# Kernel optimization log

Hardware: AMD Instinct MI355X
Metric: run time of the kernel (lower is better)

## Reference

```python
import jax, jax.numpy as jnp
import numpy as np

N, E, D, L = 32768, 65536, 128, 8

def setup_inputs() -> dict:
    key = jax.random.key(0)
    ks = jax.random.split(key, 32)
    def rn(i, shape, s=0.05):
        return jax.random.normal(ks[i], shape, dtype=jnp.float32) * s
    inp = dict(
        hs_init=rn(0, (N, D), 1.0),
        edge_index=jax.random.randint(ks[1], (2, E), 0, N, dtype=jnp.int32),
        gate=jax.random.randint(ks[2], (N,), 0, 3, dtype=jnp.int32),
        level=jax.random.randint(ks[3], (N,), 0, L + 1, dtype=jnp.int32),
        gcn_w=rn(4, (D, D)), gcn_b=rn(5, (D,)),
        mu_w=rn(6, (D, D)), mu_b=rn(7, (D,)),
        ls_w=rn(8, (D, D)), ls_b=rn(9, (D,)),
        as_w=rn(10, (D, D)), as_b=rn(11, (D,)),
        ns_w=rn(12, (D, D)), ns_b=rn(13, (D,)),
        af_w=rn(14, (2 * D, D)), af_b=rn(15, (D,)),
        nf_w=rn(16, (D, D)), nf_b=rn(17, (D,)),
        ua_w=rn(18, (2 * D, D)), ua_b=rn(19, (D,)),
        un_w=rn(20, (D, D)), un_b=rn(21, (D,)),
        dec_ws=rn(22, (D, D)), dec_wt=rn(23, (D, D)),
    )
    return inp

def reference(hs_init, edge_index, gate, level, gcn_w, gcn_b, mu_w, mu_b, ls_w, ls_b,
              as_w, as_b, ns_w, ns_b, af_w, af_b, nf_w, nf_b, ua_w, ua_b, un_w, un_b,
              dec_ws, dec_wt):
    seg = jax.ops.segment_sum
    src, dst = edge_index[0], edge_index[1]
    n = hs_init.shape[0]
    hs = hs_init                       # structural embedding [N, D]
    hf = jnp.zeros_like(hs)            # functional embedding [N, D]
    and_mask = gate == 1
    not_mask = gate == 2
    # --- GCN encoder (self-loops, symmetric in-degree normalization) ---
    x = hs @ gcn_w
    deg = seg(jnp.ones_like(src, dtype=x.dtype), dst, num_segments=n) + 1.0
    dis = jax.lax.rsqrt(deg)
    coef = (dis[src] * dis[dst])[:, None]
    x = seg(coef * x[src], dst, num_segments=n) + (1.0 / deg)[:, None] * x + gcn_b
    # --- VAE head: eval mode -> hs = mu (logstd computed as in module, unused) ---
    mu = x @ mu_w + mu_b
    logstd = jnp.minimum(x @ ls_w + ls_b, 10.0)  # MAX_LOGSTD clamp, eval-mode unused
    hs = mu
    # --- level-wise propagation: gather -> MLP aggr (sum) -> masked scatter update ---
    for l in range(1, L + 1):
        lvl = level == l
        # AND gates at this level
        m_and = and_mask & lvl
        e_and = m_and[dst].astype(hs.dtype)[:, None]   # edges targeting level-l ANDs
        msg = jax.nn.relu(hs @ as_w + as_b)
        agg = seg(e_and * msg[src], dst, num_segments=n)
        hs_and = jax.nn.relu(jnp.concatenate([hs, agg], axis=1) @ ua_w + ua_b)
        hs = jnp.where(m_and[:, None], hs_and, hs)
        fmsg = jax.nn.relu(jnp.concatenate([hs, hf], axis=1) @ af_w + af_b)
        fagg = seg(e_and * fmsg[src], dst, num_segments=n)
        hf = jnp.where(m_and[:, None], fagg, hf)
        # NOT gates at this level
        m_not = not_mask & lvl
        e_not = m_not[dst].astype(hs.dtype)[:, None]
        msg = jax.nn.relu(hs @ ns_w + ns_b)
        agg = seg(e_not * msg[src], dst, num_segments=n)
        hs_not = jnp.tanh(agg @ un_w + un_b)
        hs = jnp.where(m_not[:, None], hs_not, hs)
        fmsg = jax.nn.relu(hf @ nf_w + nf_b)
        fagg = seg(e_not * fmsg[src], dst, num_segments=n)
        hf = jnp.where(m_not[:, None], fagg, hf)
    # --- directed inner-product decoder -> node-level functional embedding ---
    zs = hs @ dec_ws
    zt = hs @ dec_wt
    w = jax.nn.sigmoid(jnp.sum(zs[src] * zt[dst], axis=-1))[:, None]  # [E,1]
    hf = seg(w * zs[src], dst, num_segments=n)
    return hs, hf
```

## Files before the change

### kernel.cpp

```cpp
#include <hip/hip_runtime.h>

#define DIM 128
#define NLEV 8
#define NB_STAGE 512
#define NSLOT (NB_STAGE * 4)
#define CAP NSLOT

#define AS4 0
#define UA4 4096
#define NS4 12288
#define UN4 16384
#define PACK4_TOTAL 20480
#define DEC_TOTAL 16384

__device__ __forceinline__ int cls_of(int g, int l) {
    if (l < 1 || l > NLEV) return -1;
    if (g == 1) return l - 1;
    if (g == 2) return NLEV + (l - 1);
    return -1;
}


__global__ __launch_bounds__(256) void count_kernel(const int* __restrict__ dstv,
                                                    int* __restrict__ degi, int E,
                                                    const int* __restrict__ gate,
                                                    const int* __restrict__ level,
                                                    int* __restrict__ nlist,
                                                    int* __restrict__ ncnt,
                                                    int* __restrict__ clsidx, int n) {
    const int i = blockIdx.x * 256 + threadIdx.x;
    if (i < E) atomicAdd(&degi[dstv[i]], 1);
    if ((int)blockIdx.x * 256 < n) {
        __shared__ int lcnt[16];
        __shared__ int lbase[16];
        const int t = threadIdx.x;
        if (t < 16) lcnt[t] = 0;
        __syncthreads();
        int c = -1, lpos = 0;
        if (i < n) {
            c = cls_of(gate[i], level[i]);
            if (c >= 0) lpos = atomicAdd(&lcnt[c], 1);
        }
        __syncthreads();
        if (t < 16 && lcnt[t] > 0) lbase[t] = atomicAdd(&ncnt[t], lcnt[t]);
        __syncthreads();
        if (c >= 0) {
            int idx = lbase[c] + lpos;
            nlist[c * n + idx] = i;
            clsidx[i] = (c << 16) | idx;
        }
    }
}

__global__ void pack_kernel(const float* __restrict__ as_w, const float* __restrict__ ua_w,
                            const float* __restrict__ ns_w, const float* __restrict__ un_w,
                            float4* __restrict__ wp4,
                            const float* __restrict__ ws_w, const float* __restrict__ wt_w,
                            float2* __restrict__ wdec,
                            const float* __restrict__ gcn_b, const float* __restrict__ mu_w,
                            const float* __restrict__ mu_b, float* __restrict__ bp) {
    if (blockIdx.x == gridDim.x - 1) {
        const int j = threadIdx.x;
        if (j < DIM) {
            float acc = mu_b[j];
            for (int k = 0; k < DIM; k++) acc = fmaf(gcn_b[k], mu_w[k * DIM + j], acc);
            bp[j] = acc;
        }
        return;
    }
    const int i = blockIdx.x * 256 + threadIdx.x;
    if (i < PACK4_TOTAL) {
        const float* src;
        int local;
        if (i < UA4)      { src = as_w; local = i; }
        else if (i < NS4) { src = ua_w; local = i - UA4; }
        else if (i < UN4) { src = ns_w; local = i - NS4; }
        else              { src = un_w; local = i - UN4; }
        const int kp = local >> 6, jl = local & 63;
        wp4[i] = make_float4(src[(2 * kp) * DIM + jl], src[(2 * kp) * DIM + jl + 64],
                             src[(2 * kp + 1) * DIM + jl], src[(2 * kp + 1) * DIM + jl + 64]);
    } else if (i < PACK4_TOTAL + DEC_TOTAL) {
        const int d = i - PACK4_TOTAL;
        wdec[d] = make_float2(ws_w[d], wt_w[d]);
    }
}

__global__ __launch_bounds__(1024) void scan1_kernel(const int* __restrict__ degi,
                                                     int* __restrict__ offs,
                                                     int* __restrict__ bsum,
                                                     float* __restrict__ dis,
                                                     float* __restrict__ inv) {
    __shared__ int sh[1024];
    const int gid = blockIdx.x * 1024 + threadIdx.x;
    const int v = degi[gid];
    {
        float d = (float)v + 1.0f;
        dis[gid] = rsqrtf(d);
        inv[gid] = 1.0f / d;
    }
    sh[threadIdx.x] = v;
    __syncthreads();
    for (int off = 1; off < 1024; off <<= 1) {
        int t = (threadIdx.x >= off) ? sh[threadIdx.x - off] : 0;
        __syncthreads();
        sh[threadIdx.x] += t;
        __syncthreads();
    }
    offs[gid] = sh[threadIdx.x] - v;
    if (threadIdx.x == 1023) bsum[blockIdx.x] = sh[1023];
}

__global__ __launch_bounds__(1024) void scan3_kernel(int* __restrict__ offs,
                                                     const int* __restrict__ bsum, int n) {
    __shared__ int sbase, stot;
    const int nb = gridDim.x;
    if (threadIdx.x < 64) {
        const int lane = threadIdx.x;
        const int orig = (lane < nb) ? bsum[lane] : 0;
        int v = orig;
#pragma unroll
        for (int off = 1; off < 64; off <<= 1) {
            int t = __shfl_up(v, off, 64);
            if (lane >= off) v += t;
        }
        if (lane == (int)blockIdx.x) sbase = v - orig;
        if (lane == nb - 1) stot = v;
    }
    __syncthreads();
    const int gid = blockIdx.x * 1024 + threadIdx.x;
    offs[gid] += sbase;
    if (gid == n - 1) offs[n] = stot;
}

__global__ void csr_fill_kernel(const int* __restrict__ srcv, const int* __restrict__ dstv,
                                const int* __restrict__ offs, int* __restrict__ cursor,
                                int* __restrict__ csr_src, int E) {
    int i = blockIdx.x * blockDim.x + threadIdx.x;
    if (i >= E) return;
    int d = dstv[i];
    int pos = offs[d] + atomicAdd(&cursor[d], 1);
    csr_src[pos] = srcv[i];
}

template <int BIAS>
__global__ __launch_bounds__(256) void mm_kernel(const float* __restrict__ in0,
                                                 const float* __restrict__ W,
                                                 const float* __restrict__ b,
                                                 float* __restrict__ out, int n) {
    const int R = 32;
    __shared__ float tile[R * DIM];
    const size_t row0 = (size_t)blockIdx.x * R;
    for (int t = threadIdx.x; t < R * DIM / 4; t += 256)
        ((float4*)tile)[t] = ((const float4*)(in0 + row0 * DIM))[t];
    __syncthreads();
    const int g = threadIdx.x >> 7;
    const int j = threadIdx.x & 127;
    float acc[16];
#pragma unroll
    for (int r = 0; r < 16; r++) acc[r] = 0.f;
    const float* tb = tile + (g * 16) * DIM;
    for (int k = 0; k < DIM; k += 4) {
        float w0 = W[(k + 0) * DIM + j];
        float w1 = W[(k + 1) * DIM + j];
        float w2 = W[(k + 2) * DIM + j];
        float w3 = W[(k + 3) * DIM + j];
#pragma unroll
        for (int r = 0; r < 16; r++) {
            const float4 a = *reinterpret_cast<const float4*>(tb + r * DIM + k);
            acc[r] = fmaf(a.x, w0, acc[r]);
            acc[r] = fmaf(a.y, w1, acc[r]);
            acc[r] = fmaf(a.z, w2, acc[r]);
            acc[r] = fmaf(a.w, w3, acc[r]);
        }
    }
    float bias = BIAS ? b[j] : 0.f;
#pragma unroll
    for (int r = 0; r < 16; r++) out[(row0 + g * 16 + r) * DIM + j] = acc[r] + bias;
}

__global__ __launch_bounds__(256) void mm2_kernel(const float* __restrict__ in0,
                                                  const float2* __restrict__ Wd,
                                                  float* __restrict__ zs,
                                                  float* __restrict__ zt, int n) {
    const int R = 32;
    __shared__ float tile[R * DIM];
    const size_t row0 = (size_t)blockIdx.x * R;
    for (int t = threadIdx.x; t < R * DIM / 4; t += 256)
        ((float4*)tile)[t] = ((const float4*)(in0 + row0 * DIM))[t];
    __syncthreads();
    const int g = threadIdx.x >> 7;
    const int j = threadIdx.x & 127;
    float accs[16], acct[16];
#pragma unroll
    for (int r = 0; r < 16; r++) { accs[r] = 0.f; acct[r] = 0.f; }
    const float* tb = tile + (g * 16) * DIM;
    float2 s0 = Wd[0 * DIM + j], s1 = Wd[1 * DIM + j];
    float2 s2 = Wd[2 * DIM + j], s3 = Wd[3 * DIM + j];
    for (int k = 0; k < DIM; k += 2) {
        const int kn = (k + 4 < DIM) ? (k + 4) : 0;
        const float2 p0 = Wd[(kn + 0) * DIM + j];
        const float2 p1 = Wd[(kn + 1) * DIM + j];
#pragma unroll
        for (int r = 0; r < 16; r++) {
            const float2 a = *reinterpret_cast<const float2*>(tb + r * DIM + k);
            accs[r] = fmaf(a.x, s0.x, accs[r]);
            acct[r] = fmaf(a.x, s0.y, acct[r]);
            accs[r] = fmaf(a.y, s1.x, accs[r]);
            acct[r] = fmaf(a.y, s1.y, acct[r]);
        }
        s0 = s2; s1 = s3; s2 = p0; s3 = p1;
    }
#pragma unroll
    for (int r = 0; r < 16; r++) {
        zs[(row0 + g * 16 + r) * DIM + j] = accs[r];
        zt[(row0 + g * 16 + r) * DIM + j] = acct[r];
    }
}

__global__ __launch_bounds__(256) void gcn_gather_kernel(const float* __restrict__ x,
                                                         const float* __restrict__ dis,
                                                         const float* __restrict__ inv,
                                                         const int* __restrict__ offs,
                                                         const int* __restrict__ csr_src,
                                                         float* __restrict__ y, int n) {
    int slot = threadIdx.x >> 7, j = threadIdx.x & 127;
    for (int node = blockIdx.x * 2 + slot; node < n; node += gridDim.x * 2) {
        float di = dis[node];
        float acc = inv[node] * x[(size_t)node * DIM + j];
        int e1 = offs[node + 1];
        for (int p = offs[node]; p < e1; p++) {
            int s = csr_src[p];
            acc += di * dis[s] * x[(size_t)s * DIM + j];
        }
        y[(size_t)node * DIM + j] = acc;
    }
}


__device__ __forceinline__ void stage_pk(const float4* __restrict__ Wp, float4* __restrict__ W2) {
    for (int t = threadIdx.x; t < 4096; t += 256) W2[t] = Wp[t];
}

template <bool MERGE>
__device__ __forceinline__ const float* resolve_row(const float* __restrict__ base,
                                                    const float* __restrict__ tmp,
                                                    const int* __restrict__ clsidx,
                                                    int mcls, int s) {
    if (MERGE) {
        int cc = clsidx[s];
        if ((cc >> 16) == mcls && (cc & 0xFFFF) < CAP) return tmp + (size_t)(cc & 0xFFFF) * DIM;
    }
    return base + (size_t)s * DIM;
}

template <bool MERGE>
__device__ __forceinline__ void load_pair(const float* __restrict__ hs,
                                          const float* __restrict__ tmp,
                                          const int* __restrict__ clsidx, int mcls,
                                          const int* __restrict__ csr_src,
                                          int p, int e1, int lane,
                                          float& a00, float& a01, float& a10, float& a11) {
    const int s0 = csr_src[p];
    const int s1 = (p + 1 < e1) ? csr_src[p + 1] : s0;
    const float* r0 = resolve_row<MERGE>(hs, tmp, clsidx, mcls, s0);
    const float* r1 = resolve_row<MERGE>(hs, tmp, clsidx, mcls, s1);
    a00 = r0[lane]; a01 = r0[lane + 64];
    a10 = r1[lane]; a11 = r1[lane + 64];
}

__device__ __forceinline__ void mv128(const float* __restrict__ ar, const float4* __restrict__ W2,
                                      int lane, float& o0, float& o1) {
#pragma unroll 8
    for (int k = 0; k < 128; k += 4) {
        const float4 a = *(const float4*)&ar[k];
        const float4 wA = W2[(k >> 1) * 64 + lane];
        const float4 wB = W2[((k >> 1) + 1) * 64 + lane];
        o0 = fmaf(a.x, wA.x, o0); o1 = fmaf(a.x, wA.y, o1);
        o0 = fmaf(a.y, wA.z, o0); o1 = fmaf(a.y, wA.w, o1);
        o0 = fmaf(a.z, wB.x, o0); o1 = fmaf(a.z, wB.y, o1);
        o0 = fmaf(a.w, wB.z, o0); o1 = fmaf(a.w, wB.w, o1);
    }
}

template <bool MERGE>
__global__ __launch_bounds__(256) void and_stage_kernel(
        float* __restrict__ hs, const float* __restrict__ tmpN, float* __restrict__ tmpA,
        const int* __restrict__ offs, const int* __restrict__ csr_src,
        const int* __restrict__ nlist, const int* __restrict__ ncnt,
        const int* __restrict__ clsidx, const float4* __restrict__ wp4,
        const float* __restrict__ as_b, const float* __restrict__ ua_b,
        int cA, int cNp, int n) {
    const int cnt = min(ncnt[cA], CAP);
    const int cntp = MERGE ? min(ncnt[cNp], CAP) : 0;
    const int lim = max(cnt, cntp);
    if ((int)blockIdx.x * 4 >= lim) return;
    __shared__ float4 W2[4096];
    __shared__ float arow[4][256];
    const int lane = threadIdx.x & 63;
    const int wv = threadIdx.x >> 6;
    const int gslot = (blockIdx.x << 2) | wv;

    const bool act = gslot < cnt;
    const int nd = act ? nlist[cA * n + gslot] : 0;
    const int e0 = act ? offs[nd] : 0;
    const int e1 = act ? offs[nd + 1] : 0;
    float h0 = 0.f, h1 = 0.f;
    if (act) {
        h0 = hs[(size_t)nd * DIM + lane];
        h1 = hs[(size_t)nd * DIM + lane + 64];
    }
    float pa0 = 0.f, pa1 = 0.f, pa2 = 0.f, pa3 = 0.f;
    if (act && e0 < e1)
        load_pair<MERGE>(hs, tmpN, clsidx, cNp, csr_src, e0, e1, lane, pa0, pa1, pa2, pa3);
    if (MERGE) {
        for (int idx = gslot; idx < cntp; idx += NSLOT) {
            const int node = nlist[cNp * n + idx];
            hs[(size_t)node * DIM + lane] = tmpN[(size_t)idx * DIM + lane];
            hs[(size_t)node * DIM + lane + 64] = tmpN[(size_t)idx * DIM + lane + 64];
        }
    }
    stage_pk(wp4 + AS4, W2);
    __syncthreads();

    const float bj_as0 = as_b[lane], bj_as1 = as_b[lane + 64];
    float ag0 = 0.f, ag1 = 0.f;
    if (act) {
        float* ar = arow[wv];
        float a00 = pa0, a01 = pa1, a10 = pa2, a11 = pa3;
        for (int p = e0; p < e1; p += 2) {
            ar[lane] = a00; ar[64 + lane] = a01;
            ar[128 + lane] = a10; ar[192 + lane] = a11;
            const bool two = (p + 1 < e1);
            float n00 = 0.f, n01 = 0.f, n10 = 0.f, n11 = 0.f;
            if (p + 2 < e1)
                load_pair<MERGE>(hs, tmpN, clsidx, cNp, csr_src, p + 2, e1, lane,
                                 n00, n01, n10, n11);
            float m00 = bj_as0, m01 = bj_as1, m10 = bj_as0, m11 = bj_as1;
#pragma unroll 8
            for (int k = 0; k < 128; k += 4) {
                const float4 a0 = *(const float4*)&ar[k];
                const float4 a1 = *(const float4*)&ar[128 + k];
                const float4 wA = W2[(k >> 1) * 64 + lane];
                const float4 wB = W2[((k >> 1) + 1) * 64 + lane];
                m00 = fmaf(a0.x, wA.x, m00); m01 = fmaf(a0.x, wA.y, m01);
                m10 = fmaf(a1.x, wA.x, m10); m11 = fmaf(a1.x, wA.y, m11);
                m00 = fmaf(a0.y, wA.z, m00); m01 = fmaf(a0.y, wA.w, m01);
                m10 = fmaf(a1.y, wA.z, m10); m11 = fmaf(a1.y, wA.w, m11);
                m00 = fmaf(a0.z, wB.x, m00); m01 = fmaf(a0.z, wB.y, m01);
                m10 = fmaf(a1.z, wB.x, m10); m11 = fmaf(a1.z, wB.y, m11);
                m00 = fmaf(a0.w, wB.z, m00); m01 = fmaf(a0.w, wB.w, m01);
                m10 = fmaf(a1.w, wB.z, m10); m11 = fmaf(a1.w, wB.w, m11);
            }
            ag0 += fmaxf(m00, 0.f);
            ag1 += fmaxf(m01, 0.f);
            if (two) { ag0 += fmaxf(m10, 0.f); ag1 += fmaxf(m11, 0.f); }
            a00 = n00; a01 = n01; a10 = n10; a11 = n11;
        }
    }

    float u0 = ua_b[lane], u1 = ua_b[lane + 64];
    __syncthreads();
    stage_pk(wp4 + UA4, W2);
    __syncthreads();
    if (act) {
        float* ar = arow[wv];
        ar[lane] = h0; ar[64 + lane] = h1;
        mv128(ar, W2, lane, u0, u1);
    }
    __syncthreads();
    stage_pk(wp4 + UA4 + 4096, W2);
    __syncthreads();
    if (act) {
        float* ar = arow[wv];
        ar[lane] = ag0; ar[64 + lane] = ag1;
        mv128(ar, W2, lane, u0, u1);
        tmpA[(size_t)gslot * DIM + lane] = fmaxf(u0, 0.f);
        tmpA[(size_t)gslot * DIM + lane + 64] = fmaxf(u1, 0.f);
    }
}

__global__ __launch_bounds__(256) void not_stage_kernel(
        float* __restrict__ hs, const float* __restrict__ tmpA, float* __restrict__ tmpN,
        const int* __restrict__ offs, const int* __restrict__ csr_src,
        const int* __restrict__ nlist, const int* __restrict__ ncnt,
        const int* __restrict__ clsidx, const float4* __restrict__ wp4,
        const float* __restrict__ ns_b, const float* __restrict__ un_b,
        int cA, int cN, int n) {
    const int cnt = min(ncnt[cN], CAP);
    const int cntA = min(ncnt[cA], CAP);
    const int lim = max(cnt, cntA);
    if ((int)blockIdx.x * 4 >= lim) return;
    __shared__ float4 W2[4096];
    __shared__ float arow[4][256];
    const int lane = threadIdx.x & 63;
    const int wv = threadIdx.x >> 6;
    const int gslot = (blockIdx.x << 2) | wv;

    const bool act = gslot < cnt;
    const int nd = act ? nlist[cN * n + gslot] : 0;
    const int e0 = act ? offs[nd] : 0;
    const int e1 = act ? offs[nd + 1] : 0;
    float pa0 = 0.f, pa1 = 0.f, pa2 = 0.f, pa3 = 0.f;
    if (act && e0 < e1)
        load_pair<true>(hs, tmpA, clsidx, cA, csr_src, e0, e1, lane, pa0, pa1, pa2, pa3);
    for (int idx = gslot; idx < cntA; idx += NSLOT) {
        const int node = nlist[cA * n + idx];
        hs[(size_t)node * DIM + lane] = tmpA[(size_t)idx * DIM + lane];
        hs[(size_t)node * DIM + lane + 64] = tmpA[(size_t)idx * DIM + lane + 64];
    }
    stage_pk(wp4 + NS4, W2);
    __syncthreads();

    const float bj_ns0 = ns_b[lane], bj_ns1 = ns_b[lane + 64];
    float ag0 = 0.f, ag1 = 0.f;
    if (act) {
        float* ar = arow[wv];
        float a00 = pa0, a01 = pa1, a10 = pa2, a11 = pa3;
        for (int p = e0; p < e1; p += 2) {
            ar[lane] = a00; ar[64 + lane] = a01;
            ar[128 + lane] = a10; ar[192 + lane] = a11;
            const bool two = (p + 1 < e1);
            float n00 = 0.f, n01 = 0.f, n10 = 0.f, n11 = 0.f;
            if (p + 2 < e1)
                load_pair<true>(hs, tmpA, clsidx, cA, csr_src, p + 2, e1, lane,
                                n00, n01, n10, n11);
            float m00 = bj_ns0, m01 = bj_ns1, m10 = bj_ns0, m11 = bj_ns1;
#pragma unroll 8
            for (int k = 0; k < 128; k += 4) {
                const float4 a0 = *(const float4*)&ar[k];
                const float4 a1 = *(const float4*)&ar[128 + k];
                const float4 wA = W2[(k >> 1) * 64 + lane];
                const float4 wB = W2[((k >> 1) + 1) * 64 + lane];
                m00 = fmaf(a0.x, wA.x, m00); m01 = fmaf(a0.x, wA.y, m01);
                m10 = fmaf(a1.x, wA.x, m10); m11 = fmaf(a1.x, wA.y, m11);
                m00 = fmaf(a0.y, wA.z, m00); m01 = fmaf(a0.y, wA.w, m01);
                m10 = fmaf(a1.y, wA.z, m10); m11 = fmaf(a1.y, wA.w, m11);
                m00 = fmaf(a0.z, wB.x, m00); m01 = fmaf(a0.z, wB.y, m01);
                m10 = fmaf(a1.z, wB.x, m10); m11 = fmaf(a1.z, wB.y, m11);
                m00 = fmaf(a0.w, wB.z, m00); m01 = fmaf(a0.w, wB.w, m01);
                m10 = fmaf(a1.w, wB.z, m10); m11 = fmaf(a1.w, wB.w, m11);
            }
            ag0 += fmaxf(m00, 0.f);
            ag1 += fmaxf(m01, 0.f);
            if (two) { ag0 += fmaxf(m10, 0.f); ag1 += fmaxf(m11, 0.f); }
            a00 = n00; a01 = n01; a10 = n10; a11 = n11;
        }
    }

    float u0 = un_b[lane], u1 = un_b[lane + 64];
    __syncthreads();
    stage_pk(wp4 + UN4, W2);
    __syncthreads();
    if (act) {
        float* ar = arow[wv];
        ar[lane] = ag0; ar[64 + lane] = ag1;
        mv128(ar, W2, lane, u0, u1);
        tmpN[(size_t)gslot * DIM + lane] = tanhf(u0);
        tmpN[(size_t)gslot * DIM + lane + 64] = tanhf(u1);
    }
}

__global__ __launch_bounds__(256) void commit_kernel(float* __restrict__ hs,
                                                     const float* __restrict__ tmp,
                                                     const int* __restrict__ nlist,
                                                     const int* __restrict__ ncnt,
                                                     int c, int n) {
    const int lane = threadIdx.x & 63;
    const int gslot = (blockIdx.x << 2) | (threadIdx.x >> 6);
    const int cnt = min(ncnt[c], CAP);
    for (int idx = gslot; idx < cnt; idx += NSLOT) {
        const int node = nlist[c * n + idx];
        hs[(size_t)node * DIM + lane] = tmp[(size_t)idx * DIM + lane];
        hs[(size_t)node * DIM + lane + 64] = tmp[(size_t)idx * DIM + lane + 64];
    }
}

__global__ __launch_bounds__(256) void dec_gather_kernel(const float* __restrict__ zs,
                                                         const float* __restrict__ zt,
                                                         const int* __restrict__ offs,
                                                         const int* __restrict__ csr_src,
                                                         float* __restrict__ hf_out, int n) {
    int w = threadIdx.x >> 6, lane = threadIdx.x & 63;
    for (int node = blockIdx.x * 4 + w; node < n; node += gridDim.x * 4) {
        float b0 = zt[(size_t)node * DIM + lane];
        float b1 = zt[(size_t)node * DIM + 64 + lane];
        float acc0 = 0.f, acc1 = 0.f;
        int e1 = offs[node + 1];
        for (int p = offs[node]; p < e1; p++) {
            int s = csr_src[p];
            float a0 = zs[(size_t)s * DIM + lane];
            float a1 = zs[(size_t)s * DIM + 64 + lane];
            float pd = a0 * b0 + a1 * b1;
#pragma unroll
            for (int off = 32; off > 0; off >>= 1) pd += __shfl_xor(pd, off, 64);
            float wg = 1.f / (1.f + __expf(-pd));
            acc0 += wg * a0;
            acc1 += wg * a1;
        }
        hf_out[(size_t)node * DIM + lane] = acc0;
        hf_out[(size_t)node * DIM + 64 + lane] = acc1;
    }
}

extern "C" void kernel_launch(void* const* d_in, const int* in_sizes, int n_in,
                              void* d_out, int out_size, void* d_ws, size_t ws_size,
                              hipStream_t stream) {
    const float* hs_init = (const float*)d_in[0];
    const int* ei = (const int*)d_in[1];
    const int* gate = (const int*)d_in[2];
    const int* level = (const int*)d_in[3];
    const float* gcn_w = (const float*)d_in[4];
    const float* gcn_b = (const float*)d_in[5];
    const float* mu_w = (const float*)d_in[6];
    const float* mu_b = (const float*)d_in[7];
    const float* as_w = (const float*)d_in[10];
    const float* as_b = (const float*)d_in[11];
    const float* ns_w = (const float*)d_in[12];
    const float* ns_b = (const float*)d_in[13];
    const float* ua_w = (const float*)d_in[18];
    const float* ua_b = (const float*)d_in[19];
    const float* un_w = (const float*)d_in[20];
    const float* un_b = (const float*)d_in[21];
    const float* dec_ws_w = (const float*)d_in[22];
    const float* dec_wt_w = (const float*)d_in[23];

    const int n = in_sizes[0] / DIM;
    const int E = in_sizes[1] / 2;
    const int* srcv = ei;
    const int* dstv = ei + E;

    float* hs = (float*)d_out;
    float* hf_out = hs + (size_t)n * DIM;

    char* wp = (char*)d_ws;
    float* x = (float*)wp;      wp += (size_t)n * DIM * 4;
    float* x2 = (float*)wp;     wp += (size_t)n * DIM * 4;
    float* tmpA = (float*)wp;   wp += (size_t)CAP * DIM * 4;
    float* tmpN = (float*)wp;   wp += (size_t)CAP * DIM * 4;
    float4* wp4 = (float4*)wp;  wp += (size_t)PACK4_TOTAL * 16;
    float2* wdec = (float2*)wp; wp += (size_t)DEC_TOTAL * 8;
    float* wprime = (float*)wp; wp += (size_t)DIM * DIM * 4;
    float* bprime = (float*)wp; wp += (size_t)DIM * 4;
    char* small0 = wp;
    int* degi = (int*)wp;   wp += (size_t)n * 4;
    int* cursor = (int*)wp; wp += (size_t)n * 4;
    int* ncnt = (int*)wp;   wp += 16 * 4;
    size_t small_bytes = (size_t)(wp - small0);
    int* bsum = (int*)wp;    wp += 64 * 4;
    int* offs = (int*)wp;    wp += (size_t)(n + 1) * 4;
    int* csr_src = (int*)wp; wp += (size_t)E * 4;
    int* nlist = (int*)wp;   wp += (size_t)16 * n * 4;
    int* clsidx = (int*)wp;  wp += (size_t)n * 4;
    float* dis = (float*)wp; wp += (size_t)n * 4;
    float* inv = (float*)wp; wp += (size_t)n * 4;

    hipMemsetAsync(small0, 0, small_bytes, stream);
    hipMemsetAsync(clsidx, 0xFF, (size_t)n * 4, stream);

    mm_kernel<0><<<DIM / 32, 256, 0, stream>>>(gcn_w, mu_w, nullptr, wprime, DIM);
    pack_kernel<<<(PACK4_TOTAL + DEC_TOTAL + 255) / 256 + 1, 256, 0, stream>>>(
        as_w, ua_w, ns_w, un_w, wp4, dec_ws_w, dec_wt_w, wdec, gcn_b, mu_w, mu_b, bprime);

    count_kernel<<<(E + 255) / 256, 256, 0, stream>>>(dstv, degi, E, gate, level,
                                                      nlist, ncnt, clsidx, n);
    scan1_kernel<<<n / 1024, 1024, 0, stream>>>(degi, offs, bsum, dis, inv);
    scan3_kernel<<<n / 1024, 1024, 0, stream>>>(offs, bsum, n);
    csr_fill_kernel<<<(E + 255) / 256, 256, 0, stream>>>(srcv, dstv, offs, cursor, csr_src, E);

    gcn_gather_kernel<<<4096, 256, 0, stream>>>(hs_init, dis, inv, offs, csr_src, x, n);
    mm_kernel<1><<<n / 32, 256, 0, stream>>>(x, wprime, bprime, hs, n);

    for (int l = 1; l <= NLEV; l++) {
        const int cA = l - 1;
        const int cN = NLEV + l - 1;
        const int cNp = NLEV + l - 2;
        if (l == 1)
            and_stage_kernel<false><<<NB_STAGE, 256, 0, stream>>>(
                hs, tmpN, tmpA, offs, csr_src, nlist, ncnt, clsidx, wp4,
                as_b, ua_b, cA, -9, n);
        else
            and_stage_kernel<true><<<NB_STAGE, 256, 0, stream>>>(
                hs, tmpN, tmpA, offs, csr_src, nlist, ncnt, clsidx, wp4,
                as_b, ua_b, cA, cNp, n);
        not_stage_kernel<<<NB_STAGE, 256, 0, stream>>>(
            hs, tmpA, tmpN, offs, csr_src, nlist, ncnt, clsidx, wp4,
            ns_b, un_b, cA, cN, n);
    }
    commit_kernel<<<NB_STAGE, 256, 0, stream>>>(hs, tmpN, nlist, ncnt, 2 * NLEV - 1, n);

    float* zs = x;
    float* zt = x2;
    mm2_kernel<<<n / 32, 256, 0, stream>>>(hs, wdec, zs, zt, n);
    dec_gather_kernel<<<4096, 256, 0, stream>>>(zs, zt, offs, csr_src, hf_out, n);
}
```

Measured before the change: 447.8 us.

## Precompute AND-gate self-projection hs@ua_w for all levels before propagation

Each AND node's own hs row cannot change before its level is processed, so the self half of the update matmul (hs @ ua_w_top + bias) is hoisted into one batched tiled kernel that runs before the level loop. The per-level AND stage then reads the precomputed row instead of staging the weight and running a serial matvec, which removes one weight staging pass and two barriers per level from the critical path. It adds a workspace buffer of 8*CAP*DIM floats. Separately, the gcn and decoder gather grids are doubled.

```diff
diff --git a/kernel.cpp b/kernel.cpp
--- a/kernel.cpp
+++ b/kernel.cpp
@@ -178,6 +178,60 @@
     for (int r = 0; r < 16; r++) out[(row0 + g * 16 + r) * DIM + j] = acc[r] + bias;
 }
 
+__global__ __launch_bounds__(256) void uh_kernel(const float* __restrict__ hs,
+                                                 const float* __restrict__ ua_w,
+                                                 const float* __restrict__ ua_b,
+                                                 const int* __restrict__ nlist,
+                                                 const int* __restrict__ ncnt,
+                                                 float* __restrict__ uH, int n) {
+    const int c = blockIdx.x >> 6;
+    const int i0 = (blockIdx.x & 63) * 32;
+    const int cnt = min(ncnt[c], CAP);
+    if (i0 >= cnt) return;
+    __shared__ float tile[32 * DIM];
+    {
+        const int rt = threadIdx.x >> 3;
+        const int ct = threadIdx.x & 7;
+        const int idx = min(i0 + rt, cnt - 1);
+        const int node = nlist[c * n + idx];
+        const float4* s4 = (const float4*)(hs + (size_t)node * DIM);
+        float4* d4 = (float4*)(tile + rt * DIM);
+#pragma unroll
+        for (int i = 0; i < 4; i++) d4[ct + 8 * i] = s4[ct + 8 * i];
+    }
+    __syncthreads();
+    const int g = threadIdx.x >> 7;
+    const int j = threadIdx.x & 127;
+    float acc[16];
+#pragma unroll
+    for (int r = 0; r < 16; r++) acc[r] = 0.f;
+    const float* tb = tile + (g * 16) * DIM;
+    float w0 = ua_w[0 * DIM + j], w1 = ua_w[1 * DIM + j];
+    float w2 = ua_w[2 * DIM + j], w3 = ua_w[3 * DIM + j];
+    for (int k = 0; k < DIM; k += 4) {
+        const int kn = (k + 4 < DIM) ? (k + 4) : 0;
+        const float nw0 = ua_w[(kn + 0) * DIM + j];
+        const float nw1 = ua_w[(kn + 1) * DIM + j];
+        const float nw2 = ua_w[(kn + 2) * DIM + j];
+        const float nw3 = ua_w[(kn + 3) * DIM + j];
+#pragma unroll
+        for (int r = 0; r < 16; r++) {
+            const float4 a = *reinterpret_cast<const float4*>(tb + r * DIM + k);
+            acc[r] = fmaf(a.x, w0, acc[r]);
+            acc[r] = fmaf(a.y, w1, acc[r]);
+            acc[r] = fmaf(a.z, w2, acc[r]);
+            acc[r] = fmaf(a.w, w3, acc[r]);
+        }
+        w0 = nw0; w1 = nw1; w2 = nw2; w3 = nw3;
+    }
+    const float bj = ua_b[j];
+#pragma unroll
+    for (int r = 0; r < 16; r++) {
+        const int idx = i0 + g * 16 + r;
+        if (idx < cnt) uH[((size_t)c * CAP + idx) * DIM + j] = acc[r] + bj;
+    }
+}
+
 __global__ __launch_bounds__(256) void mm2_kernel(const float* __restrict__ in0,
                                                   const float2* __restrict__ Wd,
                                                   float* __restrict__ zs,
@@ -288,7 +342,7 @@
         const int* __restrict__ offs, const int* __restrict__ csr_src,
         const int* __restrict__ nlist, const int* __restrict__ ncnt,
         const int* __restrict__ clsidx, const float4* __restrict__ wp4,
-        const float* __restrict__ as_b, const float* __restrict__ ua_b,
+        const float* __restrict__ as_b, const float* __restrict__ uH,
         int cA, int cNp, int n) {
     const int cnt = min(ncnt[cA], CAP);
     const int cntp = MERGE ? min(ncnt[cNp], CAP) : 0;
@@ -304,10 +358,10 @@
     const int nd = act ? nlist[cA * n + gslot] : 0;
     const int e0 = act ? offs[nd] : 0;
     const int e1 = act ? offs[nd + 1] : 0;
-    float h0 = 0.f, h1 = 0.f;
+    float u0 = 0.f, u1 = 0.f;
     if (act) {
-        h0 = hs[(size_t)nd * DIM + lane];
-        h1 = hs[(size_t)nd * DIM + lane + 64];
+        u0 = uH[((size_t)cA * CAP + gslot) * DIM + lane];
+        u1 = uH[((size_t)cA * CAP + gslot) * DIM + lane + 64];
     }
     float pa0 = 0.f, pa1 = 0.f, pa2 = 0.f, pa3 = 0.f;
     if (act && e0 < e1)
@@ -358,15 +412,6 @@
         }
     }
 
-    float u0 = ua_b[lane], u1 = ua_b[lane + 64];
-    __syncthreads();
-    stage_pk(wp4 + UA4, W2);
-    __syncthreads();
-    if (act) {
-        float* ar = arow[wv];
-        ar[lane] = h0; ar[64 + lane] = h1;
-        mv128(ar, W2, lane, u0, u1);
-    }
     __syncthreads();
     stage_pk(wp4 + UA4 + 4096, W2);
     __syncthreads();
@@ -537,6 +582,7 @@
     float* x2 = (float*)wp;     wp += (size_t)n * DIM * 4;
     float* tmpA = (float*)wp;   wp += (size_t)CAP * DIM * 4;
     float* tmpN = (float*)wp;   wp += (size_t)CAP * DIM * 4;
+    float* uH = (float*)wp;     wp += (size_t)8 * CAP * DIM * 4;
     float4* wp4 = (float4*)wp;  wp += (size_t)PACK4_TOTAL * 16;
     float2* wdec = (float2*)wp; wp += (size_t)DEC_TOTAL * 8;
     float* wprime = (float*)wp; wp += (size_t)DIM * DIM * 4;
@@ -567,8 +613,10 @@
     scan3_kernel<<<n / 1024, 1024, 0, stream>>>(offs, bsum, n);
     csr_fill_kernel<<<(E + 255) / 256, 256, 0, stream>>>(srcv, dstv, offs, cursor, csr_src, E);
 
-    gcn_gather_kernel<<<4096, 256, 0, stream>>>(hs_init, dis, inv, offs, csr_src, x, n);
+    gcn_gather_kernel<<<8192, 256, 0, stream>>>(hs_init, dis, inv, offs, csr_src, x, n);
     mm_kernel<1><<<n / 32, 256, 0, stream>>>(x, wprime, bprime, hs, n);
+
+    uh_kernel<<<8 * 64, 256, 0, stream>>>(hs, ua_w, ua_b, nlist, ncnt, uH, n);
 
     for (int l = 1; l <= NLEV; l++) {
         const int cA = l - 1;
@@ -577,11 +625,11 @@
         if (l == 1)
             and_stage_kernel<false><<<NB_STAGE, 256, 0, stream>>>(
                 hs, tmpN, tmpA, offs, csr_src, nlist, ncnt, clsidx, wp4,
-                as_b, ua_b, cA, -9, n);
+                as_b, uH, cA, -9, n);
         else
             and_stage_kernel<true><<<NB_STAGE, 256, 0, stream>>>(
                 hs, tmpN, tmpA, offs, csr_src, nlist, ncnt, clsidx, wp4,
-                as_b, ua_b, cA, cNp, n);
+                as_b, uH, cA, cNp, n);
         not_stage_kernel<<<NB_STAGE, 256, 0, stream>>>(
             hs, tmpA, tmpN, offs, csr_src, nlist, ncnt, clsidx, wp4,
             ns_b, un_b, cA, cN, n);
@@ -591,5 +639,5 @@
     float* zs = x;
     float* zt = x2;
     mm2_kernel<<<n / 32, 256, 0, stream>>>(hs, wdec, zs, zt, n);
-    dec_gather_kernel<<<4096, 256, 0, stream>>>(zs, zt, offs, csr_src, hf_out, n);
-}
+    dec_gather_kernel<<<8192, 256, 0, stream>>>(zs, zt, offs, csr_src, hf_out, n);
+}
```

Measured after the change: 440.4 us. About the same (-1.7%).
